# Kernel optimization log

Measured on AMD Instinct MI355X. Metric: run time of the kernel, lower is better.

The kernel has to match this reference:

```python
import jax, jax.numpy as jnp
import numpy as np

NUM_USERS = 100000
NUM_ITEMS = 100000
EMB_DIM = 64
NUM_NODES = NUM_USERS + NUM_ITEMS
NUM_EDGES = 4000000
BATCH = 4096
NUM_LAYERS = 2


def setup_inputs() -> dict:
    key = jax.random.key(0)
    ks = jax.random.split(key, 8)
    user = jax.random.randint(ks[0], (BATCH,), 0, NUM_USERS, dtype=jnp.int64) if jax.config.jax_enable_x64 else jax.random.randint(ks[0], (BATCH,), 0, NUM_USERS, dtype=jnp.int32)
    pos = jax.random.randint(ks[1], (BATCH,), 0, NUM_ITEMS, dtype=jnp.int32)
    neg = jax.random.randint(ks[2], (BATCH,), 0, NUM_ITEMS, dtype=jnp.int32)
    edge_row = jax.random.randint(ks[3], (NUM_EDGES,), 0, NUM_NODES, dtype=jnp.int32)
    edge_col = jax.random.randint(ks[4], (NUM_EDGES,), 0, NUM_NODES, dtype=jnp.int32)
    # normalized adjacency values (degree-normalized in real LightGCN)
    edge_val = jax.random.uniform(ks[5], (NUM_EDGES,), dtype=jnp.float32) * 0.01
    user_emb = jax.random.normal(ks[6], (NUM_USERS, EMB_DIM), dtype=jnp.float32) * 0.01
    item_emb = jax.random.normal(ks[7], (NUM_ITEMS, EMB_DIM), dtype=jnp.float32) * 0.01
    return {"user": user, "pos": pos, "neg": neg,
            "edge_row": edge_row, "edge_col": edge_col, "edge_val": edge_val,
            "user_emb": user_emb, "item_emb": item_emb}


def _spmm(edge_row, edge_col, edge_val, x):
    # out[r] = sum_e val[e] * x[col[e]]  -- sparse adjacency times dense emb
    msgs = edge_val[:, None] * x[edge_col]  # [E, D]
    return jax.ops.segment_sum(msgs, edge_row, num_segments=NUM_NODES)


def reference(user, pos, neg, edge_row, edge_col, edge_val, user_emb, item_emb):
    all_emb = jnp.concatenate([user_emb, item_emb], axis=0)  # [N, D]
    acc = all_emb
    h = all_emb
    for _ in range(NUM_LAYERS):
        h = _spmm(edge_row, edge_col, edge_val, h)
        acc = acc + h
    lightgcn_out = acc / (NUM_LAYERS + 1)  # mean over stacked layer embeddings
    u = lightgcn_out[:NUM_USERS]
    i = lightgcn_out[NUM_USERS:]
    user_latent = u[user]          # [B, D]
    positive_latent = i[pos]       # [B, D]
    negative_latent = i[neg]       # [B, D]
    positive_score = jnp.sum(user_latent * positive_latent, axis=1)
    negative_score = jnp.sum(user_latent * negative_latent, axis=1)
    return positive_score, negative_score
```

## Files before the change

kernel.cpp:

```cpp
#include <hip/hip_runtime.h>
#include <cstdint>
#include <cstddef>

#define NUM_USERS 100000
#define NUM_ITEMS 100000
#define NUM_NODES 200000
#define NUM_EDGES 4000000
#define BATCH     4096
#define EMB       64

#define NB    782
#define CAP   5632
#define CHUNK 16384
#define PTHREADS 1024
#define EPB   16


__device__ __forceinline__ unsigned short f2bf(float f) {
    unsigned u = __float_as_uint(f);
    u = (u + 0x7FFFu + ((u >> 16) & 1u)) >> 16;
    return (unsigned short)u;
}
__device__ __forceinline__ float bf2f(unsigned short b) {
    return __uint_as_float(((unsigned)b) << 16);
}


__global__ void k_cvt(const float* __restrict__ uemb, const float* __restrict__ iemb,
                      unsigned short* __restrict__ xb, int* __restrict__ bcur) {
    int i = blockIdx.x * blockDim.x + threadIdx.x;
    if (i < NB) bcur[i] = i * CAP;
    const int TOT8 = (NUM_NODES * EMB) / 8;
    if (i >= TOT8) return;
    size_t off = (size_t)i * 8;
    const size_t UELEMS = (size_t)NUM_USERS * EMB;
    const float* src = (off < UELEMS) ? (uemb + off) : (iemb + (off - UELEMS));
    float4 f0 = ((const float4*)src)[0];
    float4 f1 = ((const float4*)src)[1];
    ushort4 o0 = make_ushort4(f2bf(f0.x), f2bf(f0.y), f2bf(f0.z), f2bf(f0.w));
    ushort4 o1 = make_ushort4(f2bf(f1.x), f2bf(f1.y), f2bf(f1.z), f2bf(f1.w));
    ((ushort4*)(xb + off))[0] = o0;
    ((ushort4*)(xb + off))[1] = o1;
}


__global__ void k_part1(const int* __restrict__ erow, const int* __restrict__ ecol,
                        const float* __restrict__ eval_, int* __restrict__ bcur,
                        int2* __restrict__ tmp) {
    __shared__ int hist[NB];
    __shared__ int base[NB];
    int t = threadIdx.x;
    int start = blockIdx.x * CHUNK;
    for (int i = t; i < NB; i += PTHREADS) hist[i] = 0;
    __syncthreads();
    int rows[EPB], ranks[EPB];
#pragma unroll
    for (int k = 0; k < EPB; ++k) {
        int e = start + t + k * PTHREADS;
        if (e < NUM_EDGES) {
            int r = erow[e];
            rows[k]  = r;
            ranks[k] = atomicAdd(&hist[r >> 8], 1);
        } else {
            rows[k] = -1;
        }
    }
    __syncthreads();
    for (int i = t; i < NB; i += PTHREADS) {
        int c = hist[i];
        base[i] = c ? atomicAdd(&bcur[i], c) : 0;
    }
    __syncthreads();
#pragma unroll
    for (int k = 0; k < EPB; ++k) {
        int e = start + t + k * PTHREADS;
        if (rows[k] >= 0) {
            int r   = rows[k];
            int bkt = r >> 8;
            int pos = base[bkt] + ranks[k];
            if (pos < (bkt + 1) * CAP)
                tmp[pos] = make_int2(((r & 255) << 24) | ecol[e], __float_as_int(eval_[e]));
        }
    }
}


__global__ void k_part2(const int* __restrict__ bcur, const int2* __restrict__ tmp,
                        int2* __restrict__ epack, int2* __restrict__ rowext) {
    __shared__ int cnt[256];
    __shared__ int sc[256];
    __shared__ int loc[256];
    int b = blockIdx.x, t = threadIdx.x;
    int base_row = b << 8;
    int nrows = min(256, NUM_NODES - base_row);
    int s0 = b * CAP;
    int n = min(bcur[b] - s0, CAP);
    if (t < 256) cnt[t] = 0;
    __syncthreads();
    for (int i = t; i < n; i += 512)
        atomicAdd(&cnt[((unsigned)tmp[s0 + i].x) >> 24], 1);
    __syncthreads();
    int v = 0;
    if (t < 256) { v = cnt[t]; sc[t] = v; }
    __syncthreads();
    for (int off = 1; off < 256; off <<= 1) {
        int add = 0;
        if (t < 256 && t >= off) add = sc[t - off];
        __syncthreads();
        if (t < 256 && t >= off) sc[t] += add;
        __syncthreads();
    }
    if (t < 256) {
        int cur = s0 + sc[t] - v;
        if (t < nrows) rowext[base_row + t] = make_int2(cur, v);
        loc[t] = cur;
    }
    __syncthreads();
    for (int i = t; i < n; i += 512) {
        int2 rec = tmp[s0 + i];
        int pos = atomicAdd(&loc[((unsigned)rec.x) >> 24], 1);
        epack[pos] = make_int2(rec.x & 0xFFFFFF, rec.y);
    }
}


__global__ void k_spmm1(const int2* __restrict__ rowext, const int2* __restrict__ epack,
                        const unsigned short* __restrict__ xb,
                        unsigned short* __restrict__ h1) {
    int wid  = (blockIdx.x * blockDim.x + threadIdx.x) >> 6;
    int lane = threadIdx.x & 63;
    if (wid >= NUM_NODES) return;
    int g = lane >> 4;
    int q = (lane & 15) * 4;
    int2 se = rowext[wid];
    int s = se.x, t = se.x + se.y;
    float a0 = 0.f, a1 = 0.f, a2 = 0.f, a3 = 0.f;
    for (int e = s; e < t; e += 8) {
        int eA = e + g, eB = e + 4 + g;
        int2 pA = epack[eA < t ? eA : s];
        int2 pB = epack[eB < t ? eB : s];
        float vA = (eA < t) ? __int_as_float(pA.y) : 0.f;
        float vB = (eB < t) ? __int_as_float(pB.y) : 0.f;
        ushort4 xA = *(const ushort4*)(xb + (size_t)pA.x * EMB + q);
        ushort4 xB = *(const ushort4*)(xb + (size_t)pB.x * EMB + q);
        a0 = fmaf(vA, bf2f(xA.x), a0); a1 = fmaf(vA, bf2f(xA.y), a1);
        a2 = fmaf(vA, bf2f(xA.z), a2); a3 = fmaf(vA, bf2f(xA.w), a3);
        a0 = fmaf(vB, bf2f(xB.x), a0); a1 = fmaf(vB, bf2f(xB.y), a1);
        a2 = fmaf(vB, bf2f(xB.z), a2); a3 = fmaf(vB, bf2f(xB.w), a3);
    }
    a0 += __shfl_xor(a0, 16, 64); a1 += __shfl_xor(a1, 16, 64);
    a2 += __shfl_xor(a2, 16, 64); a3 += __shfl_xor(a3, 16, 64);
    a0 += __shfl_xor(a0, 32, 64); a1 += __shfl_xor(a1, 32, 64);
    a2 += __shfl_xor(a2, 32, 64); a3 += __shfl_xor(a3, 32, 64);
    if (lane < 16) {
        ushort4 o = make_ushort4(f2bf(a0), f2bf(a1), f2bf(a2), f2bf(a3));
        *(ushort4*)(h1 + (size_t)wid * EMB + q) = o;
    }
}


__device__ __forceinline__ const float* node_ptr(int c, const float* __restrict__ uemb,
                                                 const float* __restrict__ iemb) {
    return (c < NUM_USERS) ? (uemb + (size_t)c * EMB)
                           : (iemb + (size_t)(c - NUM_USERS) * EMB);
}

__global__ void k_final(const int* __restrict__ user, const int* __restrict__ pos,
                        const int* __restrict__ neg,
                        const int2* __restrict__ rowext, const int2* __restrict__ epack,
                        const float* __restrict__ uemb, const float* __restrict__ iemb,
                        const unsigned short* __restrict__ h1, float* __restrict__ out) {
    __shared__ float lds[3 * EMB];
    int b    = blockIdx.x;
    int w    = threadIdx.x >> 6;
    int lane = threadIdx.x & 63;
    int g = lane >> 4;
    int q = (lane & 15) * 4;

    int node;
    if (w == 0)      node = user[b];
    else if (w == 1) node = NUM_USERS + pos[b];
    else             node = NUM_USERS + neg[b];

    int2 se = rowext[node];
    int s = se.x, t = se.x + se.y;
    float a0 = 0.f, a1 = 0.f, a2 = 0.f, a3 = 0.f;
    for (int e = s; e < t; e += 8) {
        int eA = e + g, eB = e + 4 + g;
        int2 pA = epack[eA < t ? eA : s];
        int2 pB = epack[eB < t ? eB : s];
        float vA = (eA < t) ? __int_as_float(pA.y) : 0.f;
        float vB = (eB < t) ? __int_as_float(pB.y) : 0.f;
        ushort4 yA = *(const ushort4*)(h1 + (size_t)pA.x * EMB + q);
        ushort4 yB = *(const ushort4*)(h1 + (size_t)pB.x * EMB + q);
        a0 = fmaf(vA, bf2f(yA.x), a0); a1 = fmaf(vA, bf2f(yA.y), a1);
        a2 = fmaf(vA, bf2f(yA.z), a2); a3 = fmaf(vA, bf2f(yA.w), a3);
        a0 = fmaf(vB, bf2f(yB.x), a0); a1 = fmaf(vB, bf2f(yB.y), a1);
        a2 = fmaf(vB, bf2f(yB.z), a2); a3 = fmaf(vB, bf2f(yB.w), a3);
    }
    a0 += __shfl_xor(a0, 16, 64); a1 += __shfl_xor(a1, 16, 64);
    a2 += __shfl_xor(a2, 16, 64); a3 += __shfl_xor(a3, 16, 64);
    a0 += __shfl_xor(a0, 32, 64); a1 += __shfl_xor(a1, 32, 64);
    a2 += __shfl_xor(a2, 32, 64); a3 += __shfl_xor(a3, 32, 64);

    if (lane < 16) {
        const float* xbp = node_ptr(node, uemb, iemb) + q;
        float4  xd = *(const float4*)xbp;
        ushort4 hn = *(const ushort4*)(h1 + (size_t)node * EMB + q);
        a0 = (a0 + xd.x + bf2f(hn.x)) / 3.0f;
        a1 = (a1 + xd.y + bf2f(hn.y)) / 3.0f;
        a2 = (a2 + xd.z + bf2f(hn.z)) / 3.0f;
        a3 = (a3 + xd.w + bf2f(hn.w)) / 3.0f;
        *(float4*)(lds + w * EMB + q) = make_float4(a0, a1, a2, a3);
    }
    __syncthreads();

    if (w < 2) {
        float prod = lds[lane] * lds[(w + 1) * EMB + lane];
        for (int off = 32; off; off >>= 1) prod += __shfl_xor(prod, off, 64);
        if (lane == 0) out[w * BATCH + b] = prod;
    }
}


extern "C" void kernel_launch(void* const* d_in, const int* in_sizes, int n_in,
                              void* d_out, int out_size, void* d_ws, size_t ws_size,
                              hipStream_t stream) {
    const int*   user  = (const int*)d_in[0];
    const int*   pos   = (const int*)d_in[1];
    const int*   neg   = (const int*)d_in[2];
    const int*   erow  = (const int*)d_in[3];
    const int*   ecol  = (const int*)d_in[4];
    const float* eval_ = (const float*)d_in[5];
    const float* uemb  = (const float*)d_in[6];
    const float* iemb  = (const float*)d_in[7];
    float* out = (float*)d_out;

    char* ws = (char*)d_ws;
    unsigned short* xb = (unsigned short*)(ws);
    unsigned short* h1 = (unsigned short*)(ws + 25600000);
    int2* tmp     = (int2*)(ws + 25600000);
    int2* rowext  = (int2*)(ws + 60833792);
    int*  bcur    = (int*)(ws + 62433792);
    int2* epack   = (int2*)(ws + 62437888);

    k_cvt<<<((NUM_NODES * EMB) / 8 + 255) / 256, 256, 0, stream>>>(uemb, iemb, xb, bcur);

    k_part1<<<(NUM_EDGES + CHUNK - 1) / CHUNK, PTHREADS, 0, stream>>>(erow, ecol, eval_,
                                                                      bcur, tmp);

    k_part2<<<NB, 512, 0, stream>>>(bcur, tmp, epack, rowext);

    k_spmm1<<<(NUM_NODES * 64 + 255) / 256, 256, 0, stream>>>(rowext, epack, xb, h1);

    k_final<<<BATCH, 192, 0, stream>>>(user, pos, neg, rowext, epack,
                                       uemb, iemb, h1, out);
}
```

Baseline: 343.0 us.

## Fold fp32-to-bf16 conversion into partition kernel and use 512-row buckets

```diff
diff --git a/kernel.cpp b/kernel.cpp
--- a/kernel.cpp
+++ b/kernel.cpp
@@ -9,11 +9,13 @@
 #define BATCH     4096
 #define EMB       64
 
-#define NB    782
-#define CAP   5632
+#define RPB   512
+#define NB    391
+#define CAP   11264
 #define CHUNK 16384
 #define PTHREADS 1024
 #define EPB   16
+
 
 
 __device__ __forceinline__ unsigned short f2bf(float f) {
@@ -23,24 +25,6 @@
 }
 __device__ __forceinline__ float bf2f(unsigned short b) {
     return __uint_as_float(((unsigned)b) << 16);
-}
-
-
-__global__ void k_cvt(const float* __restrict__ uemb, const float* __restrict__ iemb,
-                      unsigned short* __restrict__ xb, int* __restrict__ bcur) {
-    int i = blockIdx.x * blockDim.x + threadIdx.x;
-    if (i < NB) bcur[i] = i * CAP;
-    const int TOT8 = (NUM_NODES * EMB) / 8;
-    if (i >= TOT8) return;
-    size_t off = (size_t)i * 8;
-    const size_t UELEMS = (size_t)NUM_USERS * EMB;
-    const float* src = (off < UELEMS) ? (uemb + off) : (iemb + (off - UELEMS));
-    float4 f0 = ((const float4*)src)[0];
-    float4 f1 = ((const float4*)src)[1];
-    ushort4 o0 = make_ushort4(f2bf(f0.x), f2bf(f0.y), f2bf(f0.z), f2bf(f0.w));
-    ushort4 o1 = make_ushort4(f2bf(f1.x), f2bf(f1.y), f2bf(f1.z), f2bf(f1.w));
-    ((ushort4*)(xb + off))[0] = o0;
-    ((ushort4*)(xb + off))[1] = o1;
 }
 
 
@@ -60,7 +44,7 @@
         if (e < NUM_EDGES) {
             int r = erow[e];
             rows[k]  = r;
-            ranks[k] = atomicAdd(&hist[r >> 8], 1);
+            ranks[k] = atomicAdd(&hist[r >> 9], 1);
         } else {
             rows[k] = -1;
         }
@@ -76,50 +60,65 @@
         int e = start + t + k * PTHREADS;
         if (rows[k] >= 0) {
             int r   = rows[k];
-            int bkt = r >> 8;
-            int pos = base[bkt] + ranks[k];
+            int bkt = r >> 9;
+            int pos = bkt * CAP + base[bkt] + ranks[k];
             if (pos < (bkt + 1) * CAP)
-                tmp[pos] = make_int2(((r & 255) << 24) | ecol[e], __float_as_int(eval_[e]));
+                tmp[pos] = make_int2(((r & 511) << 18) | ecol[e], __float_as_int(eval_[e]));
         }
     }
 }
 
 
 __global__ void k_part2(const int* __restrict__ bcur, const int2* __restrict__ tmp,
-                        int2* __restrict__ epack, int2* __restrict__ rowext) {
-    __shared__ int cnt[256];
-    __shared__ int sc[256];
-    __shared__ int loc[256];
+                        int2* __restrict__ epack, int2* __restrict__ rowext,
+                        const float* __restrict__ uemb, const float* __restrict__ iemb,
+                        unsigned short* __restrict__ xb) {
+    __shared__ int cnt[RPB];
+    __shared__ int sc[RPB];
+    __shared__ int loc[RPB];
     int b = blockIdx.x, t = threadIdx.x;
-    int base_row = b << 8;
-    int nrows = min(256, NUM_NODES - base_row);
+
+    const int TOT8 = (NUM_NODES * EMB) / 8;
+    const int PER  = (TOT8 + NB - 1) / NB;
+    int u0 = b * PER, u1 = min(u0 + PER, TOT8);
+    const size_t UELEMS = (size_t)NUM_USERS * EMB;
+    for (int u = u0 + t; u < u1; u += 512) {
+        size_t off = (size_t)u * 8;
+        const float* src = (off < UELEMS) ? (uemb + off) : (iemb + (off - UELEMS));
+        float4 f0 = ((const float4*)src)[0];
+        float4 f1 = ((const float4*)src)[1];
+        ushort4 o0 = make_ushort4(f2bf(f0.x), f2bf(f0.y), f2bf(f0.z), f2bf(f0.w));
+        ushort4 o1 = make_ushort4(f2bf(f1.x), f2bf(f1.y), f2bf(f1.z), f2bf(f1.w));
+        ((ushort4*)(xb + off))[0] = o0;
+        ((ushort4*)(xb + off))[1] = o1;
+    }
+
+    int base_row = b << 9;
+    int nrows = min(RPB, NUM_NODES - base_row);
     int s0 = b * CAP;
-    int n = min(bcur[b] - s0, CAP);
-    if (t < 256) cnt[t] = 0;
+    int n = min(bcur[b], CAP);
+    cnt[t] = 0;
     __syncthreads();
     for (int i = t; i < n; i += 512)
-        atomicAdd(&cnt[((unsigned)tmp[s0 + i].x) >> 24], 1);
-    __syncthreads();
-    int v = 0;
-    if (t < 256) { v = cnt[t]; sc[t] = v; }
-    __syncthreads();
-    for (int off = 1; off < 256; off <<= 1) {
-        int add = 0;
-        if (t < 256 && t >= off) add = sc[t - off];
+        atomicAdd(&cnt[((unsigned)tmp[s0 + i].x) >> 18], 1);
+    __syncthreads();
+    int v = cnt[t];
+    sc[t] = v;
+    __syncthreads();
+    for (int off = 1; off < RPB; off <<= 1) {
+        int add = (t >= off) ? sc[t - off] : 0;
         __syncthreads();
-        if (t < 256 && t >= off) sc[t] += add;
+        sc[t] += add;
         __syncthreads();
     }
-    if (t < 256) {
-        int cur = s0 + sc[t] - v;
-        if (t < nrows) rowext[base_row + t] = make_int2(cur, v);
-        loc[t] = cur;
-    }
+    int cur = s0 + sc[t] - v;
+    if (t < nrows) rowext[base_row + t] = make_int2(cur, v);
+    loc[t] = cur;
     __syncthreads();
     for (int i = t; i < n; i += 512) {
         int2 rec = tmp[s0 + i];
-        int pos = atomicAdd(&loc[((unsigned)rec.x) >> 24], 1);
-        epack[pos] = make_int2(rec.x & 0xFFFFFF, rec.y);
+        int pos = atomicAdd(&loc[((unsigned)rec.x) >> 18], 1);
+        epack[pos] = make_int2(rec.x & 0x3FFFF, rec.y);
     }
 }
 
@@ -244,12 +243,12 @@
     int*  bcur    = (int*)(ws + 62433792);
     int2* epack   = (int2*)(ws + 62437888);
 
-    k_cvt<<<((NUM_NODES * EMB) / 8 + 255) / 256, 256, 0, stream>>>(uemb, iemb, xb, bcur);
+    hipMemsetAsync(bcur, 0, NB * sizeof(int), stream);
 
     k_part1<<<(NUM_EDGES + CHUNK - 1) / CHUNK, PTHREADS, 0, stream>>>(erow, ecol, eval_,
                                                                       bcur, tmp);
 
-    k_part2<<<NB, 512, 0, stream>>>(bcur, tmp, epack, rowext);
+    k_part2<<<NB, RPB, 0, stream>>>(bcur, tmp, epack, rowext, uemb, iemb, xb);
 
     k_spmm1<<<(NUM_NODES * 64 + 255) / 256, 256, 0, stream>>>(rowext, epack, xb, h1);
 
```

Result: no change. 346.8 us (+1.1%).
